# Kernel optimization log

Hardware: AMD Instinct MI355X
Metric: run time of the kernel (lower is better)

Reference implementation:

```python
import jax, jax.numpy as jnp
import numpy as np

N_NODES = 100000
N_EDGES = 1250000
D = 64
K = 5
EPS = 1e-8


def setup_inputs() -> dict:
    key = jax.random.key(0)
    k1, k2, k3, k4 = jax.random.split(key, 4)
    x = jax.random.normal(k1, (N_NODES, D), dtype=jnp.float32)
    mask = jax.random.normal(k2, (N_NODES, 1), dtype=jnp.float32)
    edge_index = jax.random.randint(k3, (2, N_EDGES), 0, N_NODES, dtype=jnp.int64)
    # orthogonal-ish init for the linear layer (QR of gaussian), gain for tanh = 5/3
    g = jax.random.normal(k4, (D, D), dtype=jnp.float32)
    q, _ = jnp.linalg.qr(g)
    W = (5.0 / 3.0) * q.astype(jnp.float32)
    b = jnp.zeros((D,), dtype=jnp.float32)
    alpha = jnp.float32(0.001)
    return {"x": x, "mask": mask, "edge_index": edge_index, "W": W, "b": b, "alpha": alpha}


def _forward(x, mask, edge_index, W, b, alpha):
    n = x.shape[0]
    # x_fn: Linear + Tanh
    h = jnp.tanh(x @ W.T + b)  # [N, D]
    src = edge_index[0]
    dst = edge_index[1]
    hs = h[src]  # [E, D] gather
    hd = h[dst]  # [E, D] gather
    # torch cosine_similarity with eps clamp on each norm
    ns = jnp.maximum(jnp.sqrt(jnp.sum(hs * hs, axis=-1)), EPS)
    nd = jnp.maximum(jnp.sqrt(jnp.sum(hd * hd, axis=-1)), EPS)
    cos = jnp.sum(hs * hd, axis=-1) / (ns * nd)
    edge_weights = jax.nn.relu(cos)  # [E]

    # gcn_norm with self loops (PyG APPNP default): D^-1/2 (A + I) D^-1/2
    loop = jnp.arange(n, dtype=src.dtype)
    row = jnp.concatenate([src, loop])
    col = jnp.concatenate([dst, loop])
    w = jnp.concatenate([edge_weights, jnp.ones((n,), dtype=edge_weights.dtype)])
    deg = jax.ops.segment_sum(w, col, num_segments=n)
    dis = jnp.where(deg > 0, jax.lax.rsqrt(jnp.maximum(deg, EPS)), 0.0)
    norm_w = dis[row] * w * dis[col]  # [E + N]

    # APPNP: K steps of f = (1-alpha) * A_hat @ f + alpha * f0
    f0 = jax.nn.relu(mask)  # [N, 1]
    f = f0
    for _ in range(K):
        msg = norm_w[:, None] * f[row]  # gather + weight
        agg = jax.ops.segment_sum(msg, col, num_segments=n)  # scatter-add
        f = (1.0 - alpha) * agg + alpha * f0
    return f, edge_weights


def reference(x, mask, edge_index, W, b, alpha):
    return _forward(x, mask, edge_index, W, b, alpha)
```

## Files before the change

kernel.cpp:

```cpp
#include <hip/hip_runtime.h>
#include <hip/hip_fp16.h>
#include <math.h>

#define N_NODES 100000
#define N_EDGES 1250000
#define D 64
#define EPS 1e-8f

#define ZERO_BLOCKS 391
#define GEMM_BLOCKS 1024
#define NODE_BLOCKS 391
#define COSR_BLOCKS 9766

__global__ __launch_bounds__(256) void k_gemm_zero(
    const float* __restrict__ x, const float* __restrict__ W,
    const float* __restrict__ b, __half* __restrict__ hn, int* __restrict__ cnt)
{
    if (blockIdx.x < ZERO_BLOCKS) {
        int i = blockIdx.x * 256 + threadIdx.x;
        if (i < N_NODES) cnt[i] = 0;
        return;
    }
    __shared__ float xrow[4][72];
    const int lane = threadIdx.x & 63;
    const int wid  = threadIdx.x >> 6;

    float Wreg[64];
    const float4* Wv = (const float4*)(W + lane * D);
    #pragma unroll
    for (int q = 0; q < 16; ++q) {
        float4 w4 = Wv[q];
        Wreg[4*q+0] = w4.x; Wreg[4*q+1] = w4.y;
        Wreg[4*q+2] = w4.z; Wreg[4*q+3] = w4.w;
    }
    const float bj = b[lane];
    float* xl = xrow[wid];

    const int wave   = (blockIdx.x - ZERO_BLOCKS) * 4 + wid;
    const int nwaves = GEMM_BLOCKS * 4;

    for (int row = wave; row < N_NODES; row += nwaves) {
        float xv = x[(size_t)row * D + lane];
        xl[lane] = xv;
        float acc = bj;
        #pragma unroll
        for (int q = 0; q < 16; ++q) {
            float4 xk4 = *(const float4*)(xl + 4*q);
            acc = fmaf(xk4.x, Wreg[4*q+0], acc);
            acc = fmaf(xk4.y, Wreg[4*q+1], acc);
            acc = fmaf(xk4.z, Wreg[4*q+2], acc);
            acc = fmaf(xk4.w, Wreg[4*q+3], acc);
        }
        float h = tanhf(acc);
        float s = h * h;
        #pragma unroll
        for (int m = 32; m >= 1; m >>= 1) s += __shfl_xor(s, m, 64);
        float nrm = fmaxf(sqrtf(s), EPS);
        hn[(size_t)row * D + lane] = __float2half_rn(h / nrm);
    }
}

__device__ __forceinline__ float dot8h(float4 a, float4 c)
{
    const __half2* ah = (const __half2*)&a;
    const __half2* ch = (const __half2*)&c;
    float p = 0.0f;
    #pragma unroll
    for (int q = 0; q < 4; ++q) {
        float2 af = __half22float2(ah[q]);
        float2 cf = __half22float2(ch[q]);
        p = fmaf(af.x, cf.x, p);
        p = fmaf(af.y, cf.y, p);
    }
    return p;
}

__global__ __launch_bounds__(256) void k_cos_rank(
    const int* __restrict__ ei, const __half* __restrict__ hn,
    int* __restrict__ cnt, int* __restrict__ rank, float* __restrict__ wout)
{
    int t = blockIdx.x * 256 + threadIdx.x;
    int g = t >> 3, sub = t & 7;
    if (g >= N_EDGES / 4) return;
    int e0 = g * 4;
    int4 ss = *(const int4*)(ei + e0);
    int4 dd = *(const int4*)(ei + N_EDGES + e0);

    float4 a0 = ((const float4*)(hn + (size_t)ss.x * D))[sub];
    float4 c0 = ((const float4*)(hn + (size_t)dd.x * D))[sub];
    float4 a1 = ((const float4*)(hn + (size_t)ss.y * D))[sub];
    float4 c1 = ((const float4*)(hn + (size_t)dd.y * D))[sub];
    float4 a2 = ((const float4*)(hn + (size_t)ss.z * D))[sub];
    float4 c2 = ((const float4*)(hn + (size_t)dd.z * D))[sub];
    float4 a3 = ((const float4*)(hn + (size_t)ss.w * D))[sub];
    float4 c3 = ((const float4*)(hn + (size_t)dd.w * D))[sub];

    float p0 = dot8h(a0, c0);
    float p1 = dot8h(a1, c1);
    float p2 = dot8h(a2, c2);
    float p3 = dot8h(a3, c3);
    p0 += __shfl_xor(p0, 1, 64);  p1 += __shfl_xor(p1, 1, 64);
    p2 += __shfl_xor(p2, 1, 64);  p3 += __shfl_xor(p3, 1, 64);
    p0 += __shfl_xor(p0, 2, 64);  p1 += __shfl_xor(p1, 2, 64);
    p2 += __shfl_xor(p2, 2, 64);  p3 += __shfl_xor(p3, 2, 64);
    p0 += __shfl_xor(p0, 4, 64);  p1 += __shfl_xor(p1, 4, 64);
    p2 += __shfl_xor(p2, 4, 64);  p3 += __shfl_xor(p3, 4, 64);

    float w0 = fmaxf(p0, 0.0f);
    float w1 = fmaxf(p1, 0.0f);
    float w2 = fmaxf(p2, 0.0f);
    float w3 = fmaxf(p3, 0.0f);

    if (sub == 0) {
        *(float4*)(wout + e0) = make_float4(w0, w1, w2, w3);
    }
    if (sub < 4) {
        float w = (sub == 0) ? w0 : (sub == 1) ? w1 : (sub == 2) ? w2 : w3;
        int   d = (sub == 0) ? dd.x : (sub == 1) ? dd.y : (sub == 2) ? dd.z : dd.w;
        if (w > 0.0f)
            rank[e0 + sub] = atomicAdd(cnt + d, 1);
    }
}

__device__ __forceinline__ int wave_iscan(int v, int lane)
{
    int incl = v;
    #pragma unroll
    for (int m = 1; m < 64; m <<= 1) {
        int o = __shfl_up(incl, m, 64);
        if (lane >= m) incl += o;
    }
    return incl;
}

__global__ __launch_bounds__(256) void k_scan1(
    const int* __restrict__ cnt, int* __restrict__ rowptr, int* __restrict__ bsum)
{
    __shared__ int wsum[4];
    int t = threadIdx.x, b = blockIdx.x;
    int i = b * 256 + t;
    int lane = t & 63, wid = t >> 6;
    int v = (i < N_NODES) ? cnt[i] : 0;
    int incl = wave_iscan(v, lane);
    if (lane == 63) wsum[wid] = incl;
    __syncthreads();
    int off = 0;
    #pragma unroll
    for (int k = 0; k < 4; ++k) if (k < wid) off += wsum[k];
    if (i < N_NODES) rowptr[i] = off + incl - v;
    if (t == 255) bsum[b] = off + incl;
}

__global__ __launch_bounds__(512) void k_scan2(
    const int* __restrict__ bsum, int* __restrict__ boff, int nblk,
    int* __restrict__ rowptr)
{
    __shared__ int wsum[8];
    int t = threadIdx.x;
    int lane = t & 63, wid = t >> 6;
    int v = (t < nblk) ? bsum[t] : 0;
    int incl = wave_iscan(v, lane);
    if (lane == 63) wsum[wid] = incl;
    __syncthreads();
    int off = 0;
    #pragma unroll
    for (int k = 0; k < 8; ++k) if (k < wid) off += wsum[k];
    if (t < nblk) boff[t] = off + incl - v;
    if (t == nblk - 1) rowptr[N_NODES] = off + incl;
}

__global__ __launch_bounds__(256) void k_place(
    const int* __restrict__ ei, const int* __restrict__ rank_pos,
    const int* __restrict__ rowptr, const int* __restrict__ boff,
    const float* __restrict__ wsrc, int2* __restrict__ pairs)
{
    int e = blockIdx.x * 256 + threadIdx.x;
    if (e >= N_EDGES) return;
    float w = wsrc[e];
    if (!(w > 0.0f)) return;
    int s = ei[e];
    int d = ei[N_EDGES + e];
    int pos = rowptr[d] + boff[d >> 8] + rank_pos[e];
    pairs[pos] = make_int2(s, __float_as_int(w));
}

__global__ __launch_bounds__(256) void k_dis_y(
    const int* __restrict__ rowptr, const int* __restrict__ boff,
    const int2* __restrict__ pairs, const float* __restrict__ mask,
    float* __restrict__ dis, float* __restrict__ y)
{
    int t = blockIdx.x * 256 + threadIdx.x;
    int node = t >> 2, l = t & 3;
    if (node >= N_NODES) return;
    int beg = rowptr[node] + boff[node >> 8];
    int np1 = node + 1;
    int end = rowptr[np1] + (np1 < N_NODES ? boff[np1 >> 8] : 0);
    float s = 0.0f;
    for (int j = beg + l; j < end; j += 8) {
        int2 p0 = pairs[j];
        int j2 = j + 4;
        int2 p1 = make_int2(0, 0);
        if (j2 < end) p1 = pairs[j2];
        s += __int_as_float(p0.y);
        s += __int_as_float(p1.y);
    }
    s += __shfl_xor(s, 1, 64);
    s += __shfl_xor(s, 2, 64);
    if (l == 0) {
        float di = rsqrtf(fmaxf(s + 1.0f, EPS));
        dis[node] = di;
        y[node] = di * fmaxf(mask[node], 0.0f);
    }
}

__global__ __launch_bounds__(256) void k_spmv(
    const int* __restrict__ rowptr, const int* __restrict__ boff,
    const int2* __restrict__ pairs,
    const float* __restrict__ y_in, const float* __restrict__ dis,
    const float* __restrict__ mask, const float* __restrict__ alpha_p,
    float* __restrict__ y_out, float* __restrict__ f_out)
{
    int t = blockIdx.x * 256 + threadIdx.x;
    int node = t >> 2, l = t & 3;
    if (node >= N_NODES) return;
    int beg = rowptr[node] + boff[node >> 8];
    int np1 = node + 1;
    int end = rowptr[np1] + (np1 < N_NODES ? boff[np1 >> 8] : 0);
    float sum = 0.0f;
    for (int j = beg + l; j < end; j += 8) {
        int2 p0 = pairs[j];
        int j2 = j + 4;
        int2 p1 = make_int2(0, 0);
        if (j2 < end) p1 = pairs[j2];
        sum += __int_as_float(p0.y) * y_in[p0.x];
        sum += __int_as_float(p1.y) * y_in[p1.x];
    }
    sum += __shfl_xor(sum, 1, 64);
    sum += __shfl_xor(sum, 2, 64);
    if (l == 0) {
        float di = dis[node];
        float alpha = alpha_p[0];
        float f0 = fmaxf(mask[node], 0.0f);
        float fn = (1.0f - alpha) * di * (sum + y_in[node]) + alpha * f0;
        if (f_out) f_out[node] = fn;
        y_out[node] = di * fn;
    }
}

extern "C" void kernel_launch(void* const* d_in, const int* in_sizes, int n_in,
                              void* d_out, int out_size, void* d_ws, size_t ws_size,
                              hipStream_t stream)
{
    const float* x     = (const float*)d_in[0];
    const float* mask  = (const float*)d_in[1];
    const int*   ei    = (const int*)  d_in[2];
    const float* W     = (const float*)d_in[3];
    const float* b     = (const float*)d_in[4];
    const float* alpha = (const float*)d_in[5];

    float* out_f = (float*)d_out;
    float* out_w = (float*)d_out + N_NODES;

    float* ws = (float*)d_ws;
    __half* hn     = (__half*)ws;
    int2*  pairs   = (int2*) (ws + 3200000);
    int*   rank    = (int*)  (ws + 5700000);
    int*   cnt     = (int*)  (ws + 6950000);
    int*   rowptr  = (int*)  (ws + 7050000);
    float* dis     =          ws + 7150016;
    float* y_a     =          ws + 7250016;
    float* y_b     =          ws + 7350016;
    int*   bsum    = (int*)  (ws + 7550016);
    int*   boff    = (int*)  (ws + 7550528);

    const int edgeBlocks = (N_EDGES + 255) / 256;
    const int segBlocks  = (int)(((long long)N_NODES * 4 + 255) / 256);

    k_gemm_zero<<<ZERO_BLOCKS + GEMM_BLOCKS, 256, 0, stream>>>(x, W, b, hn, cnt);
    k_cos_rank<<<COSR_BLOCKS, 256, 0, stream>>>(ei, hn, cnt, rank, out_w);
    k_scan1<<<NODE_BLOCKS, 256, 0, stream>>>(cnt, rowptr, bsum);
    k_scan2<<<1, 512, 0, stream>>>(bsum, boff, NODE_BLOCKS, rowptr);
    k_place<<<edgeBlocks, 256, 0, stream>>>(ei, rank, rowptr, boff, out_w, pairs);
    k_dis_y<<<segBlocks, 256, 0, stream>>>(rowptr, boff, pairs, mask, dis, y_a);

    k_spmv<<<segBlocks, 256, 0, stream>>>(rowptr, boff, pairs, y_a, dis, mask, alpha, y_b, (float*)nullptr);
    k_spmv<<<segBlocks, 256, 0, stream>>>(rowptr, boff, pairs, y_b, dis, mask, alpha, y_a, (float*)nullptr);
    k_spmv<<<segBlocks, 256, 0, stream>>>(rowptr, boff, pairs, y_a, dis, mask, alpha, y_b, (float*)nullptr);
    k_spmv<<<segBlocks, 256, 0, stream>>>(rowptr, boff, pairs, y_b, dis, mask, alpha, y_a, (float*)nullptr);
    k_spmv<<<segBlocks, 256, 0, stream>>>(rowptr, boff, pairs, y_a, dis, mask, alpha, y_b, out_f);
}
```

Before: 208.1 us.

## Pack degree sum with edge count in 64-bit atomic and drop k_dis_y

The per-node edge count and the fixed-point weighted degree are packed into one 64-bit atomicAdd: the count sits in the upper 24 bits and the weight, scaled by 2^32, in the lower 40 bits. The scan kernel then computes dis and the initial y directly from this packed value, so the separate k_dis_y pass that re-read the CSR pairs is removed. This saves one kernel launch and one segmented read of the pairs array. In exchange the degree is summed in fixed point with truncation, and the 40-bit field can overflow at high in-degrees.

```diff
diff --git a/kernel.cpp b/kernel.cpp
--- a/kernel.cpp
+++ b/kernel.cpp
@@ -14,11 +14,12 @@
 
 __global__ __launch_bounds__(256) void k_gemm_zero(
     const float* __restrict__ x, const float* __restrict__ W,
-    const float* __restrict__ b, __half* __restrict__ hn, int* __restrict__ cnt)
+    const float* __restrict__ b, __half* __restrict__ hn,
+    unsigned long long* __restrict__ cnt64)
 {
     if (blockIdx.x < ZERO_BLOCKS) {
         int i = blockIdx.x * 256 + threadIdx.x;
-        if (i < N_NODES) cnt[i] = 0;
+        if (i < N_NODES) cnt64[i] = 0ULL;
         return;
     }
     __shared__ float xrow[4][72];
@@ -77,7 +78,8 @@
 
 __global__ __launch_bounds__(256) void k_cos_rank(
     const int* __restrict__ ei, const __half* __restrict__ hn,
-    int* __restrict__ cnt, int* __restrict__ rank, float* __restrict__ wout)
+    unsigned long long* __restrict__ cnt64, int* __restrict__ rank,
+    float* __restrict__ wout)
 {
     int t = blockIdx.x * 256 + threadIdx.x;
     int g = t >> 3, sub = t & 7;
@@ -117,8 +119,12 @@
     if (sub < 4) {
         float w = (sub == 0) ? w0 : (sub == 1) ? w1 : (sub == 2) ? w2 : w3;
         int   d = (sub == 0) ? dd.x : (sub == 1) ? dd.y : (sub == 2) ? dd.z : dd.w;
-        if (w > 0.0f)
-            rank[e0 + sub] = atomicAdd(cnt + d, 1);
+        if (w > 0.0f) {
+            unsigned long long pack =
+                (1ULL << 40) | (unsigned long long)(w * 4294967296.0f);
+            unsigned long long old = atomicAdd(cnt64 + d, pack);
+            rank[e0 + sub] = (int)(old >> 40);
+        }
     }
 }
 
@@ -134,13 +140,22 @@
 }
 
 __global__ __launch_bounds__(256) void k_scan1(
-    const int* __restrict__ cnt, int* __restrict__ rowptr, int* __restrict__ bsum)
+    const unsigned long long* __restrict__ cnt64, int* __restrict__ rowptr,
+    int* __restrict__ bsum, const float* __restrict__ mask,
+    float* __restrict__ dis, float* __restrict__ y)
 {
     __shared__ int wsum[4];
     int t = threadIdx.x, b = blockIdx.x;
     int i = b * 256 + t;
     int lane = t & 63, wid = t >> 6;
-    int v = (i < N_NODES) ? cnt[i] : 0;
+    unsigned long long pv = (i < N_NODES) ? cnt64[i] : 0ULL;
+    int v = (int)(pv >> 40);
+    if (i < N_NODES) {
+        float degsum = (float)(pv & 0xFFFFFFFFFFULL) * 2.3283064365386963e-10f;
+        float di = rsqrtf(fmaxf(degsum + 1.0f, EPS));
+        dis[i] = di;
+        y[i] = di * fmaxf(mask[i], 0.0f);
+    }
     int incl = wave_iscan(v, lane);
     if (lane == 63) wsum[wid] = incl;
     __syncthreads();
@@ -182,35 +197,6 @@
     int d = ei[N_EDGES + e];
     int pos = rowptr[d] + boff[d >> 8] + rank_pos[e];
     pairs[pos] = make_int2(s, __float_as_int(w));
-}
-
-__global__ __launch_bounds__(256) void k_dis_y(
-    const int* __restrict__ rowptr, const int* __restrict__ boff,
-    const int2* __restrict__ pairs, const float* __restrict__ mask,
-    float* __restrict__ dis, float* __restrict__ y)
-{
-    int t = blockIdx.x * 256 + threadIdx.x;
-    int node = t >> 2, l = t & 3;
-    if (node >= N_NODES) return;
-    int beg = rowptr[node] + boff[node >> 8];
-    int np1 = node + 1;
-    int end = rowptr[np1] + (np1 < N_NODES ? boff[np1 >> 8] : 0);
-    float s = 0.0f;
-    for (int j = beg + l; j < end; j += 8) {
-        int2 p0 = pairs[j];
-        int j2 = j + 4;
-        int2 p1 = make_int2(0, 0);
-        if (j2 < end) p1 = pairs[j2];
-        s += __int_as_float(p0.y);
-        s += __int_as_float(p1.y);
-    }
-    s += __shfl_xor(s, 1, 64);
-    s += __shfl_xor(s, 2, 64);
-    if (l == 0) {
-        float di = rsqrtf(fmaxf(s + 1.0f, EPS));
-        dis[node] = di;
-        y[node] = di * fmaxf(mask[node], 0.0f);
-    }
 }
 
 __global__ __launch_bounds__(256) void k_spmv(
@@ -262,26 +248,25 @@
     float* out_w = (float*)d_out + N_NODES;
 
     float* ws = (float*)d_ws;
-    __half* hn     = (__half*)ws;
-    int2*  pairs   = (int2*) (ws + 3200000);
-    int*   rank    = (int*)  (ws + 5700000);
-    int*   cnt     = (int*)  (ws + 6950000);
-    int*   rowptr  = (int*)  (ws + 7050000);
-    float* dis     =          ws + 7150016;
-    float* y_a     =          ws + 7250016;
-    float* y_b     =          ws + 7350016;
-    int*   bsum    = (int*)  (ws + 7550016);
-    int*   boff    = (int*)  (ws + 7550528);
+    __half* hn    = (__half*)ws;
+    int2*  pairs  = (int2*) (ws + 3200000);
+    int*   rank   = (int*)  (ws + 5700000);
+    unsigned long long* cnt64 = (unsigned long long*)(ws + 6950000);
+    int*   rowptr = (int*)  (ws + 7150000);
+    float* dis    =          ws + 7250016;
+    float* y_a    =          ws + 7350016;
+    float* y_b    =          ws + 7450016;
+    int*   bsum   = (int*)  (ws + 7550016);
+    int*   boff   = (int*)  (ws + 7550528);
 
     const int edgeBlocks = (N_EDGES + 255) / 256;
     const int segBlocks  = (int)(((long long)N_NODES * 4 + 255) / 256);
 
-    k_gemm_zero<<<ZERO_BLOCKS + GEMM_BLOCKS, 256, 0, stream>>>(x, W, b, hn, cnt);
-    k_cos_rank<<<COSR_BLOCKS, 256, 0, stream>>>(ei, hn, cnt, rank, out_w);
-    k_scan1<<<NODE_BLOCKS, 256, 0, stream>>>(cnt, rowptr, bsum);
+    k_gemm_zero<<<ZERO_BLOCKS + GEMM_BLOCKS, 256, 0, stream>>>(x, W, b, hn, cnt64);
+    k_cos_rank<<<COSR_BLOCKS, 256, 0, stream>>>(ei, hn, cnt64, rank, out_w);
+    k_scan1<<<NODE_BLOCKS, 256, 0, stream>>>(cnt64, rowptr, bsum, mask, dis, y_a);
     k_scan2<<<1, 512, 0, stream>>>(bsum, boff, NODE_BLOCKS, rowptr);
     k_place<<<edgeBlocks, 256, 0, stream>>>(ei, rank, rowptr, boff, out_w, pairs);
-    k_dis_y<<<segBlocks, 256, 0, stream>>>(rowptr, boff, pairs, mask, dis, y_a);
 
     k_spmv<<<segBlocks, 256, 0, stream>>>(rowptr, boff, pairs, y_a, dis, mask, alpha, y_b, (float*)nullptr);
     k_spmv<<<segBlocks, 256, 0, stream>>>(rowptr, boff, pairs, y_b, dis, mask, alpha, y_a, (float*)nullptr);
```

Result: faster. 202.8 us (-2.5%).
